# Kernel optimization log

Hardware: AMD Instinct MI355X
Metric: run time of the kernel (lower is better)

The kernel has to match this reference:

```python
import jax, jax.numpy as jnp
import numpy as np

B, S, P = 16, 1024, 1024
D, H, HD = 128, 8, 16      # embed_dim, num_heads, head_dim (qkv_dim)
MS = 32                    # ms_hidden_dim
E = 524288                 # number of edges
TANH_CLIP = 10.0
TEMP = 1.0
EPS = 1e-9


def setup_inputs() -> dict:
    key = jax.random.key(0)
    ks = jax.random.split(key, 12)
    inv = lambda n: 1.0 / np.sqrt(n)
    return {
        "x1": jax.random.normal(ks[0], (B, S, D), jnp.float32),
        "x2": jax.random.normal(ks[1], (B, P, D), jnp.float32),
        "b_idx": jax.random.randint(ks[2], (E,), 0, B, jnp.int32),
        "s_idx": jax.random.randint(ks[3], (E,), 0, S, jnp.int32),
        "p_idx": jax.random.randint(ks[4], (E,), 0, P, jnp.int32),
        "w": jax.random.uniform(ks[5], (E,), jnp.float32),
        "Wqv1": jax.random.normal(ks[6], (D, 2 * D), jnp.float32) * inv(D),
        "Wkv2": jax.random.normal(ks[7], (D, 2 * D), jnp.float32) * inv(D),
        "Wo1": jax.random.normal(ks[8], (D, D), jnp.float32) * inv(D),
        "Wo2": jax.random.normal(ks[9], (D, D), jnp.float32) * inv(D),
        "msW1": jax.random.normal(ks[10], (H, 2, MS), jnp.float32) * inv(2),
        "msb1": jnp.zeros((H, MS), jnp.float32),
        "msW2": jax.random.normal(ks[11], (H, MS, 1), jnp.float32) * inv(MS),
        "msb2": jnp.zeros((H, 1), jnp.float32),
    }


def _mixed_scores(logits, w, msW1, msb1, msW2, msb2):
    # logits: [E, H], w: [E] -> per-head 2->MS->1 MLP (MatNet MixedScoreFF)
    mixed = jnp.stack([logits, jnp.broadcast_to(w[:, None], logits.shape)], axis=-1)  # [E,H,2]
    hid = jax.nn.relu(jnp.einsum('ehi,him->ehm', mixed, msW1) + msb1)  # [E,H,MS]
    out = (jnp.einsum('ehm,hmo->eho', hid, msW2) + msb2)[..., 0]       # [E,H]
    return TANH_CLIP * jnp.tanh(out) / TEMP


def _group_softmax_combine(logits, values, gid, num_groups):
    # logits: [E,H], values: [E,H,HD]; exp -> segment-sum denom -> weighted scatter
    el = jnp.exp(logits)
    denom = jax.ops.segment_sum(el, gid, num_segments=num_groups)      # [G,H]
    attn = el / (denom[gid] + EPS)                                      # [E,H]
    return jax.ops.segment_sum(attn[:, :, None] * values, gid, num_segments=num_groups)  # [G,H,HD]


def reference(x1, x2, b_idx, s_idx, p_idx, w, Wqv1, Wkv2, Wo1, Wo2, msW1, msb1, msW2, msb2):
    qv1 = (x1 @ Wqv1).reshape(B, S, 2, H, HD)   # [B,S,2,H,HD]
    kv2 = (x2 @ Wkv2).reshape(B, P, 2, H, HD)
    row_flat = b_idx * S + s_idx                # [E]
    col_flat = b_idx * P + p_idx
    qv1_e = qv1.reshape(B * S, 2, H, HD)[row_flat]   # [E,2,H,HD]
    kv2_e = kv2.reshape(B * P, 2, H, HD)[col_flat]
    q, v1 = qv1_e[:, 0], qv1_e[:, 1]
    k, v2 = kv2_e[:, 0], kv2_e[:, 1]
    logits = jnp.einsum('ehd,ehd->eh', q, k) / np.sqrt(HD).astype(np.float32)
    logits = _mixed_scores(logits, w, msW1, msb1, msW2, msb2)
    row_heads = _group_softmax_combine(logits, v2, row_flat, B * S)  # [B*S,H,HD]
    col_heads = _group_softmax_combine(logits, v1, col_flat, B * P)  # [B*P,H,HD]
    h1 = row_heads.reshape(B, S, H * HD) @ Wo1
    h2 = col_heads.reshape(B, P, H * HD) @ Wo2
    return h1, h2
```

## Files before the change

### kernel.cpp

```cpp
#include <hip/hip_runtime.h>
#include <hip/hip_fp16.h>
#include <math.h>

#define BB   16
#define SS   1024
#define PP   1024
#define HH   8
#define MSS  32
#define EE   524288
#define NROW (BB*SS)
#define NCOL (BB*PP)
#define ESTRIDE 5
#define NBPX 2112
#define NB   128
#define CHUNK 4096
#define GCAP 96

__device__ __forceinline__ void gemm_tile_core(
        const float* __restrict__ Arow, const float* __restrict__ Bsrc,
        int ldb, int c0, float* As , float* Bs ,
        float4 acc4[8], int t) {
    int tx = t & 31, ty = t >> 5;
#pragma unroll
    for (int li = 0; li < 8; li++) {
        int idx = li * 256 + t;
        int r = idx >> 5, p = idx & 31;
        *(float4*)&As[r * 132 + 4 * p] = *(const float4*)(Arow + r * 128 + 4 * p);
    }
#pragma unroll
    for (int i = 0; i < 8; i++) acc4[i] = make_float4(0.f, 0.f, 0.f, 0.f);

    for (int kc = 0; kc < 4; kc++) {
        __syncthreads();
#pragma unroll
        for (int li = 0; li < 4; li++) {
            int idx = li * 256 + t;
            int kk = idx >> 5, p = idx & 31;
            *(float4*)&Bs[kk * 128 + 4 * p] =
                *(const float4*)(Bsrc + (size_t)(kc * 32 + kk) * ldb + c0 + 4 * p);
        }
        __syncthreads();
#pragma unroll
        for (int kq = 0; kq < 8; kq++) {
            float4 a4[8];
#pragma unroll
            for (int i = 0; i < 8; i++)
                a4[i] = *(const float4*)&As[(ty + 8 * i) * 132 + kc * 32 + kq * 4];
#pragma unroll
            for (int kk = 0; kk < 4; kk++) {
                float4 b4 = *(const float4*)&Bs[(kq * 4 + kk) * 128 + 4 * tx];
#pragma unroll
                for (int i = 0; i < 8; i++) {
                    float av = ((const float*)&a4[i])[kk];
                    acc4[i].x = fmaf(av, b4.x, acc4[i].x);
                    acc4[i].y = fmaf(av, b4.y, acc4[i].y);
                    acc4[i].z = fmaf(av, b4.z, acc4[i].z);
                    acc4[i].w = fmaf(av, b4.w, acc4[i].w);
                }
            }
        }
    }
}

__global__ __launch_bounds__(256) void proj_kernel(
        const float* __restrict__ x1, const float* __restrict__ x2,
        const float* __restrict__ Wqv1, const float* __restrict__ Wkv2,
        float* __restrict__ qf, float* __restrict__ kf,
        __half* __restrict__ v1h, __half* __restrict__ v2h) {
    __shared__ float As[64 * 132];
    __shared__ float Bs[32 * 128];
    int t = threadIdx.x;
    int bid = blockIdx.x;
    int matrix = bid >> 9;
    int ct = (bid >> 8) & 1;
    int mb = bid & 255;
    const float* A  = matrix ? x2 : x1;
    const float* Bm = matrix ? Wkv2 : Wqv1;

    float4 acc4[8];
    gemm_tile_core(A + (size_t)mb * 64 * 128, Bm, 256, ct * 128, As, Bs, acc4, t);

    int tx = t & 31, ty = t >> 5;
    if (ct == 0) {
        float* Cq = matrix ? kf : qf;
#pragma unroll
        for (int i = 0; i < 8; i++) {
            int row = mb * 64 + ty + 8 * i;
            *(float4*)(Cq + (size_t)row * 128 + 4 * tx) = acc4[i];
        }
    } else {
        __half* Cv = matrix ? v2h : v1h;
#pragma unroll
        for (int i = 0; i < 8; i++) {
            int row = mb * 64 + ty + 8 * i;
            __half2* p = (__half2*)(Cv + (size_t)row * 128 + 4 * tx);
            p[0] = __halves2half2(__float2half(acc4[i].x), __float2half(acc4[i].y));
            p[1] = __halves2half2(__float2half(acc4[i].z), __float2half(acc4[i].w));
        }
    }
}

__global__ __launch_bounds__(256) void outp_kernel(
        const float* __restrict__ rh, const float* __restrict__ ch,
        const float* __restrict__ Wo1, const float* __restrict__ Wo2,
        float* __restrict__ out) {
    __shared__ float As[64 * 132];
    __shared__ float Bs[32 * 128];
    int t = threadIdx.x;
    int matrix = blockIdx.x >> 8;
    int mb = blockIdx.x & 255;
    const float* A  = matrix ? ch : rh;
    const float* Bm = matrix ? Wo2 : Wo1;
    float* C = out + (size_t)matrix * NROW * 128;

    float4 acc4[8];
    gemm_tile_core(A + (size_t)mb * 64 * 128, Bm, 128, 0, As, Bs, acc4, t);

    int tx = t & 31, ty = t >> 5;
#pragma unroll
    for (int i = 0; i < 8; i++) {
        int row = mb * 64 + ty + 8 * i;
        *(float4*)(C + (size_t)row * 128 + 4 * tx) = acc4[i];
    }
}

__global__ __launch_bounds__(1024) void hist_kernel(
        const int* __restrict__ b_idx, const int* __restrict__ s_idx,
        const int* __restrict__ p_idx, unsigned int* __restrict__ ph) {
    __shared__ unsigned int lh[16384];
    int t = threadIdx.x;
#pragma unroll
    for (int i = 0; i < 16; i++) lh[t + 1024 * i] = 0;
    __syncthreads();
    int base = blockIdx.x * CHUNK;
#pragma unroll
    for (int k = 0; k < 4; k++) {
        int e = base + k * 1024 + t;
        int b = b_idx[e];
        int rbin = (b << 10) + s_idx[e];
        int cbin = 16384 + (b << 10) + p_idx[e];
        atomicAdd(&lh[rbin >> 1], 1u << (16 * (rbin & 1)));
        atomicAdd(&lh[cbin >> 1], 1u << (16 * (cbin & 1)));
    }
    __syncthreads();
    unsigned int* dst = ph + (size_t)blockIdx.x * 16384;
#pragma unroll
    for (int i = 0; i < 16; i++) dst[t + 1024 * i] = lh[t + 1024 * i];
}

__global__ __launch_bounds__(128) void scan1_kernel(
        const unsigned int* __restrict__ ph, int* __restrict__ pbase,
        int* __restrict__ tot) {
    int bin = blockIdx.x * 128 + threadIdx.x;
    int word = bin >> 1;
    int sh = 16 * (bin & 1);
    int run = 0;
#pragma unroll 8
    for (int j = 0; j < NB; j++) {
        unsigned int v = ph[(size_t)j * 16384 + word];
        pbase[(size_t)j * 32768 + bin] = run;
        run += (v >> sh) & 0xffff;
    }
    tot[bin] = run;
}

__global__ __launch_bounds__(1024) void scan2_kernel(
        const int* __restrict__ tot, int* __restrict__ offs) {
    __shared__ int sdata[1024];
    int side = blockIdx.x;
    int t = threadIdx.x;
    const int* c = tot + side * 16384;
    int* o = offs + side * (16384 + 1);
    int base = t * 16;
    int loc[16];
    int run = 0;
#pragma unroll
    for (int i = 0; i < 16; i++) { loc[i] = run; run += c[base + i]; }
    sdata[t] = run;
    __syncthreads();
    for (int st = 1; st < 1024; st <<= 1) {
        int v = (t >= st) ? sdata[t - st] : 0;
        __syncthreads();
        sdata[t] += v;
        __syncthreads();
    }
    int excl = sdata[t] - run;
#pragma unroll
    for (int i = 0; i < 16; i++) o[base + i] = excl + loc[i];
    if (t == 1023) o[16384] = sdata[1023];
}

__global__ __launch_bounds__(1024) void pos_kernel(
        const int* __restrict__ b_idx, const int* __restrict__ s_idx,
        const int* __restrict__ p_idx, const float* __restrict__ w,
        const int* __restrict__ pbase, const int* __restrict__ offs,
        int4* __restrict__ ebuf) {
    __shared__ int cur[16384];
    int t = threadIdx.x;
    {
        const int* src = pbase + (size_t)blockIdx.x * 32768 + 16384;
        const int* oc = offs + (16384 + 1);
#pragma unroll
        for (int i = 0; i < 16; i++) {
            int idx = t + 1024 * i;
            cur[idx] = oc[idx] + src[idx];
        }
    }
    __syncthreads();
    int base = blockIdx.x * CHUNK;
    int rowr[4], colr[4], pcr[4];
    float wr[4];
#pragma unroll
    for (int k = 0; k < 4; k++) {
        int e = base + k * 1024 + t;
        int b = b_idx[e];
        rowr[k] = (b << 10) + s_idx[e];
        colr[k] = (b << 10) + p_idx[e];
        wr[k] = w[e];
        pcr[k] = atomicAdd(&cur[colr[k]], 1);
    }
    __syncthreads();
    {
        const int* src = pbase + (size_t)blockIdx.x * 32768;
#pragma unroll
        for (int i = 0; i < 16; i++) {
            int idx = t + 1024 * i;
            cur[idx] = offs[idx] + src[idx];
        }
    }
    __syncthreads();
#pragma unroll
    for (int k = 0; k < 4; k++) {
        int pr = atomicAdd(&cur[rowr[k]], 1);
        ebuf[pr] = make_int4(rowr[k], colr[k], __float_as_int(wr[k]), pcr[k]);
    }
}

__global__ __launch_bounds__(256) void edge_kernel(
        const float* __restrict__ qf, const float* __restrict__ kf,
        const int4* __restrict__ ebuf, const int* __restrict__ offs_row,
        const float* __restrict__ msW1, const float* __restrict__ msb1,
        const float* __restrict__ msW2, const float* __restrict__ msb2,
        float* __restrict__ entr, float* __restrict__ entc) {
    __shared__ float4 sPk[8 * 33];
    __shared__ float sB2[8];
    int t = threadIdx.x;
    {
        int h = t >> 5, m = t & 31;
        sPk[h * 33 + m] = make_float4(msW1[h * 64 + m], msW1[h * 64 + 32 + m],
                                      msb1[h * 32 + m], msW2[h * 32 + m]);
    }
    if (t < 8) sB2[t] = msb2[t];
    __syncthreads();

    int x = blockIdx.x & 7;
    int r0 = blockIdx.x >> 3;
    int a0 = offs_row[x << 10],       a1 = offs_row[(x + 1) << 10];
    int b0 = offs_row[(x + 8) << 10], b1 = offs_row[(x + 9) << 10];
    int nA = a1 - a0;
    int n = nA + (b1 - b0);

    int l = t & 7;
    int sub = t >> 3;
    int hh = 2 * (l & 3) + (l >> 2);
    const float4* wp = &sPk[hh * 33];
    float bias2 = sB2[hh];

    for (int jb = r0 * 32; jb < n; jb += NBPX * 32) {
        int j = jb + sub;
        if (j < n) {
            int pos = (j < nA) ? (a0 + j) : (b0 + (j - nA));
            int4 rec = ebuf[pos];
            int row = rec.x, col = rec.y;
            float we = __int_as_float(rec.z);
            int pc = rec.w;

            const float4* qp4 = (const float4*)(qf + (size_t)row * 128);
            const float4* kp4 = (const float4*)(kf + (size_t)col * 128);
            float p0, p1, p2, p3;
            {
                float4 a = qp4[l],      k4 = kp4[l];
                p0 = fmaf(a.x, k4.x, fmaf(a.y, k4.y, fmaf(a.z, k4.z, a.w * k4.w)));
            }
            {
                float4 a = qp4[8 + l],  k4 = kp4[8 + l];
                p1 = fmaf(a.x, k4.x, fmaf(a.y, k4.y, fmaf(a.z, k4.z, a.w * k4.w)));
            }
            {
                float4 a = qp4[16 + l], k4 = kp4[16 + l];
                p2 = fmaf(a.x, k4.x, fmaf(a.y, k4.y, fmaf(a.z, k4.z, a.w * k4.w)));
            }
            {
                float4 a = qp4[24 + l], k4 = kp4[24 + l];
                p3 = fmaf(a.x, k4.x, fmaf(a.y, k4.y, fmaf(a.z, k4.z, a.w * k4.w)));
            }
            p0 += __shfl_xor(p0, 1); p0 += __shfl_xor(p0, 2);
            p1 += __shfl_xor(p1, 1); p1 += __shfl_xor(p1, 2);
            p2 += __shfl_xor(p2, 1); p2 += __shfl_xor(p2, 2);
            p3 += __shfl_xor(p3, 1); p3 += __shfl_xor(p3, 2);

            int js = l & 3;
            float dot = js == 0 ? p0 : (js == 1 ? p1 : (js == 2 ? p2 : p3));
            float logit = dot * 0.25f;

            float outv = bias2;
#pragma unroll 4
            for (int m = 0; m < MSS; m++) {
                float4 c = wp[m];
                float hid = fmaf(logit, c.x, fmaf(we, c.y, c.z));
                hid = fmaxf(hid, 0.f);
                outv = fmaf(hid, c.w, outv);
            }
            float ev = expf(10.0f * tanhf(outv));
            __half evh = __float2half(ev);

            float* er = entr + (size_t)pos * ESTRIDE;
            float* ec = entc + (size_t)pc * ESTRIDE;
            ((__half*)er)[2 + hh] = evh;
            ((__half*)ec)[2 + hh] = evh;
            if (l == 0) {
                er[0] = __int_as_float(col);
                ec[0] = __int_as_float(row);
            }
        }
    }
}

__global__ __launch_bounds__(128) void combine_kernel(
        const float* __restrict__ entr, const float* __restrict__ entc,
        const int* __restrict__ offs_row, const int* __restrict__ offs_col,
        const __half* __restrict__ v1h, const __half* __restrict__ v2h,
        float* __restrict__ row_heads, float* __restrict__ col_heads) {
    __shared__ float sE[GCAP * ESTRIDE];
    int x = blockIdx.x & 7;
    int r = blockIdx.x >> 3;
    int which = r >> 10;
    int sidx = r & 1023;
    int b = x + ((which & 1) << 3);
    int gl = (b << 10) + sidx;

    int t = threadIdx.x;
    int h = t >> 4;
    const float* ent; const __half* vals; const int* offs; float* outp;
    if (which < 2) { ent = entr; vals = v2h; offs = offs_row; outp = row_heads; }
    else           { ent = entc; vals = v1h; offs = offs_col; outp = col_heads; }
    int s = offs[gl], e_ = offs[gl + 1];
    int cnt = e_ - s;
    int cap = cnt < GCAP ? cnt : GCAP;

    const float* gsrc = ent + (size_t)s * ESTRIDE;
    for (int i = t; i < cap * ESTRIDE; i += 128) sE[i] = gsrc[i];
    __syncthreads();

    float acc = 0.f, den = 0.f;
#pragma unroll 8
    for (int i = 0; i < cap; i++) {
        const float* en = &sE[i * ESTRIDE];
        int other = __float_as_int(en[0]);
        float ev = __half2float(((const __half*)en)[2 + h]);
        float v = __half2float(vals[(size_t)other * 128 + t]);
        acc = fmaf(ev, v, acc);
        den += ev;
    }
    for (int i = cap; i < cnt; i++) {
        const float* en = gsrc + (size_t)i * ESTRIDE;
        int other = __float_as_int(en[0]);
        float ev = __half2float(((const __half*)en)[2 + h]);
        float v = __half2float(vals[(size_t)other * 128 + t]);
        acc = fmaf(ev, v, acc);
        den += ev;
    }
    outp[(size_t)gl * 128 + t] = acc / (den + 1e-9f);
}

extern "C" void kernel_launch(void* const* d_in, const int* in_sizes, int n_in,
                              void* d_out, int out_size, void* d_ws, size_t ws_size,
                              hipStream_t stream) {
    const float* x1   = (const float*)d_in[0];
    const float* x2   = (const float*)d_in[1];
    const int* b_idx  = (const int*)d_in[2];
    const int* s_idx  = (const int*)d_in[3];
    const int* p_idx  = (const int*)d_in[4];
    const float* w    = (const float*)d_in[5];
    const float* Wqv1 = (const float*)d_in[6];
    const float* Wkv2 = (const float*)d_in[7];
    const float* Wo1  = (const float*)d_in[8];
    const float* Wo2  = (const float*)d_in[9];
    const float* msW1 = (const float*)d_in[10];
    const float* msb1 = (const float*)d_in[11];
    const float* msW2 = (const float*)d_in[12];
    const float* msb2 = (const float*)d_in[13];
    float* out = (float*)d_out;

    float* qf = (float*)d_ws;
    float* kf = qf + (size_t)NROW * 128;
    __half* v1h = (__half*)(kf + (size_t)NCOL * 128);
    __half* v2h = v1h + (size_t)NROW * 128;
    float* entr = (float*)(v2h + (size_t)NCOL * 128);
    float* entc = entr + (size_t)EE * ESTRIDE;
    float* row_heads = entc + (size_t)EE * ESTRIDE;
    float* col_heads = row_heads + (size_t)NROW * 128;
    int4* ebuf = (int4*)(col_heads + (size_t)NCOL * 128);
    int* offs = (int*)(ebuf + EE);
    int* tot  = offs + 2 * (16384 + 1);
    unsigned int* ph = (unsigned int*)entc;
    int* pbase = (int*)row_heads;

    hist_kernel<<<NB, 1024, 0, stream>>>(b_idx, s_idx, p_idx, ph);
    scan1_kernel<<<256, 128, 0, stream>>>(ph, pbase, tot);
    scan2_kernel<<<2, 1024, 0, stream>>>(tot, offs);
    pos_kernel<<<NB, 1024, 0, stream>>>(b_idx, s_idx, p_idx, w, pbase, offs, ebuf);

    proj_kernel<<<1024, 256, 0, stream>>>(x1, x2, Wqv1, Wkv2, qf, kf, v1h, v2h);

    edge_kernel<<<8 * NBPX, 256, 0, stream>>>(
        qf, kf, ebuf, offs, msW1, msb1, msW2, msb2, entr, entc);

    combine_kernel<<<2 * NROW, 128, 0, stream>>>(
        entr, entc, offs, offs + (16384 + 1), v1h, v2h, row_heads, col_heads);

    outp_kernel<<<512, 256, 0, stream>>>(row_heads, col_heads, Wo1, Wo2, out);
}
```

Measured before the change: 243.5 us.

## Assign one row per wavefront in edge kernel and use fast tanh

The edge kernel now walks the CSR-sorted edges one row per wavefront: the q row is loaded into registers once and reused for every edge of that row, and only k rows are gathered per edge. The flat grid-stride loop that reloaded q for every edge is gone. The accurate tanhf/expf is also replaced with an __expf plus hardware-reciprocal approximation. Costs: load imbalance from uneven row degrees (about 32 edges per row, split across 8 lanes-groups, so idle lanes at row tails), and slightly lower accuracy, with a possible inf/NaN edge case for large outv.

Result: no change. 246.1 us (+1.1%).

```diff
diff --git a/kernel.cpp b/kernel.cpp
--- a/kernel.cpp
+++ b/kernel.cpp
@@ -11,7 +11,7 @@
 #define NROW (BB*SS)
 #define NCOL (BB*PP)
 #define ESTRIDE 5
-#define NBPX 2112
+#define NRWB 512
 #define NB   128
 #define CHUNK 4096
 #define GCAP 96
@@ -254,45 +254,50 @@
     __syncthreads();
 
     int x = blockIdx.x & 7;
-    int r0 = blockIdx.x >> 3;
-    int a0 = offs_row[x << 10],       a1 = offs_row[(x + 1) << 10];
-    int b0 = offs_row[(x + 8) << 10], b1 = offs_row[(x + 9) << 10];
-    int nA = a1 - a0;
-    int n = nA + (b1 - b0);
-
-    int l = t & 7;
-    int sub = t >> 3;
+    int ridx = blockIdx.x >> 3;
+    int wv = t >> 6;
+    int lane = t & 63;
+    int l = lane & 7;
+    int g = lane >> 3;
+
+    int rl = ridx * 4 + wv;
+    int row = ((x + ((rl >> 10) << 3)) << 10) + (rl & 1023);
+    int s = offs_row[row];
+    int cnt = offs_row[row + 1] - s;
+
     int hh = 2 * (l & 3) + (l >> 2);
     const float4* wp = &sPk[hh * 33];
     float bias2 = sB2[hh];
 
-    for (int jb = r0 * 32; jb < n; jb += NBPX * 32) {
-        int j = jb + sub;
-        if (j < n) {
-            int pos = (j < nA) ? (a0 + j) : (b0 + (j - nA));
+    const float4* qp4 = (const float4*)(qf + (size_t)row * 128);
+    float4 q0 = qp4[l], q1 = qp4[8 + l], q2 = qp4[16 + l], q3 = qp4[24 + l];
+
+    for (int j0 = 0; j0 < cnt; j0 += 8) {
+        int j = j0 + g;
+        if (j < cnt) {
+            int pos = s + j;
             int4 rec = ebuf[pos];
-            int row = rec.x, col = rec.y;
+            int col = rec.y;
             float we = __int_as_float(rec.z);
             int pc = rec.w;
 
-            const float4* qp4 = (const float4*)(qf + (size_t)row * 128);
             const float4* kp4 = (const float4*)(kf + (size_t)col * 128);
             float p0, p1, p2, p3;
             {
-                float4 a = qp4[l],      k4 = kp4[l];
-                p0 = fmaf(a.x, k4.x, fmaf(a.y, k4.y, fmaf(a.z, k4.z, a.w * k4.w)));
+                float4 k4 = kp4[l];
+                p0 = fmaf(q0.x, k4.x, fmaf(q0.y, k4.y, fmaf(q0.z, k4.z, q0.w * k4.w)));
             }
             {
-                float4 a = qp4[8 + l],  k4 = kp4[8 + l];
-                p1 = fmaf(a.x, k4.x, fmaf(a.y, k4.y, fmaf(a.z, k4.z, a.w * k4.w)));
+                float4 k4 = kp4[8 + l];
+                p1 = fmaf(q1.x, k4.x, fmaf(q1.y, k4.y, fmaf(q1.z, k4.z, q1.w * k4.w)));
             }
             {
-                float4 a = qp4[16 + l], k4 = kp4[16 + l];
-                p2 = fmaf(a.x, k4.x, fmaf(a.y, k4.y, fmaf(a.z, k4.z, a.w * k4.w)));
+                float4 k4 = kp4[16 + l];
+                p2 = fmaf(q2.x, k4.x, fmaf(q2.y, k4.y, fmaf(q2.z, k4.z, q2.w * k4.w)));
             }
             {
-                float4 a = qp4[24 + l], k4 = kp4[24 + l];
-                p3 = fmaf(a.x, k4.x, fmaf(a.y, k4.y, fmaf(a.z, k4.z, a.w * k4.w)));
+                float4 k4 = kp4[24 + l];
+                p3 = fmaf(q3.x, k4.x, fmaf(q3.y, k4.y, fmaf(q3.z, k4.z, q3.w * k4.w)));
             }
             p0 += __shfl_xor(p0, 1); p0 += __shfl_xor(p0, 2);
             p1 += __shfl_xor(p1, 1); p1 += __shfl_xor(p1, 2);
@@ -311,7 +316,9 @@
                 hid = fmaxf(hid, 0.f);
                 outv = fmaf(hid, c.w, outv);
             }
-            float ev = expf(10.0f * tanhf(outv));
+            float u  = __expf(outv + outv);
+            float th = 1.0f - 2.0f * __builtin_amdgcn_rcpf(u + 1.0f);
+            float ev = __expf(10.0f * th);
             __half evh = __float2half(ev);
 
             float* er = entr + (size_t)pos * ESTRIDE;
@@ -413,7 +420,7 @@
 
     proj_kernel<<<1024, 256, 0, stream>>>(x1, x2, Wqv1, Wkv2, qf, kf, v1h, v2h);
 
-    edge_kernel<<<8 * NBPX, 256, 0, stream>>>(
+    edge_kernel<<<8 * NRWB, 256, 0, stream>>>(
         qf, kf, ebuf, offs, msW1, msb1, msW2, msb2, entr, entc);
 
     combine_kernel<<<2 * NROW, 128, 0, stream>>>(
```
